# Performance work log

Hardware: AMD Instinct MI355X
Metric: run time of the kernel (lower is better)

The kernel has to match this reference:

```python
import jax, jax.numpy as jnp
from jax import lax
import numpy as np

HIDDEN = 128  # ConvLSTM hidden channels


def _conv(x, w, b, stride):
    # torch Conv2d(kernel=3, padding=1), NCHW / OIHW
    y = lax.conv_general_dilated(x, w, stride, [(1, 1), (1, 1)],
                                 dimension_numbers=('NCHW', 'OIHW', 'NCHW'))
    return y + b[None, :, None, None]


def _convT(x, w, b):
    # torch ConvTranspose2d(k=3, stride=(2,1), padding=1, output_padding=(1,0))
    # torch weight layout [Cin, Cout, kH, kW] -> flip spatially, swap IO
    wf = jnp.flip(w, (2, 3)).transpose(1, 0, 2, 3)
    y = lax.conv_general_dilated(x, wf, (1, 1), [(1, 2), (1, 1)],
                                 lhs_dilation=(2, 1),
                                 dimension_numbers=('NCHW', 'OIHW', 'NCHW'))
    return y + b[None, :, None, None]


def _bn(x, g, be, m, v):
    # eval-mode BatchNorm2d, eps=1e-5
    return g[None, :, None, None] * (x - m[None, :, None, None]) * lax.rsqrt(v[None, :, None, None] + 1e-5) + be[None, :, None, None]


def _lrelu(x):
    return jnp.where(x >= 0, x, 0.2 * x)


def _convlstm(e5, w, b):
    # e5: [B, 256, F, T]; scan over time with h,c state of shape [B, HIDDEN, F, 1]
    B, C, F, T = e5.shape
    xs = jnp.moveaxis(e5, 3, 0)[..., None]  # [T, B, C, F, 1]
    h0 = jnp.zeros((B, HIDDEN, F, 1), e5.dtype)

    def step(carry, xt):
        h, c = carry
        gates = _conv(jnp.concatenate([xt, h], axis=1), w, b, (1, 1))  # [B, 4H, F, 1]
        i, f, o, g = jnp.split(gates, 4, axis=1)
        c = jax.nn.sigmoid(f) * c + jax.nn.sigmoid(i) * jnp.tanh(g)
        h = jax.nn.sigmoid(o) * jnp.tanh(c)
        return (h, c), h

    _, hs = lax.scan(step, (h0, h0), xs)  # hs: [T, B, H, F, 1]
    return jnp.moveaxis(hs[..., 0], 0, 3)  # [B, H, F, T]


def _forward(x, enc1_w, enc1_b, enc1_g, enc1_be, enc1_m, enc1_v, enc2_w, enc2_b, enc2_g, enc2_be, enc2_m, enc2_v, enc3_w, enc3_b, enc3_g, enc3_be, enc3_m, enc3_v, enc4_w, enc4_b, enc4_g, enc4_be, enc4_m, enc4_v, enc5_w, enc5_b, enc5_g, enc5_be, enc5_m, enc5_v, lstm_w, lstm_b, dec5_w, dec5_b, dec5_g, dec5_be, dec5_m, dec5_v, dec4_w, dec4_b, dec4_g, dec4_be, dec4_m, dec4_v, dec3_w, dec3_b, dec3_g, dec3_be, dec3_m, dec3_v, dec2_w, dec2_b, dec2_g, dec2_be, dec2_m, dec2_v, dec1_w, dec1_b):
    x_log = jnp.log10(x + 1e-8)
    e1 = _lrelu(_bn(_conv(x_log, enc1_w, enc1_b, (2, 1)), enc1_g, enc1_be, enc1_m, enc1_v))
    e2 = _lrelu(_bn(_conv(e1, enc2_w, enc2_b, (2, 1)), enc2_g, enc2_be, enc2_m, enc2_v))
    e3 = _lrelu(_bn(_conv(e2, enc3_w, enc3_b, (2, 1)), enc3_g, enc3_be, enc3_m, enc3_v))
    e4 = _lrelu(_bn(_conv(e3, enc4_w, enc4_b, (2, 1)), enc4_g, enc4_be, enc4_m, enc4_v))
    e5 = _lrelu(_bn(_conv(e4, enc5_w, enc5_b, (2, 1)), enc5_g, enc5_be, enc5_m, enc5_v))
    lstm_out = _convlstm(e5, lstm_w, lstm_b)  # [B, 128, 8, T]
    d5 = jax.nn.relu(_bn(_convT(lstm_out, dec5_w, dec5_b), dec5_g, dec5_be, dec5_m, dec5_v))
    d4 = jax.nn.relu(_bn(_convT(jnp.concatenate([d5, e4], 1), dec4_w, dec4_b), dec4_g, dec4_be, dec4_m, dec4_v))
    d3 = jax.nn.relu(_bn(_convT(jnp.concatenate([d4, e3], 1), dec3_w, dec3_b), dec3_g, dec3_be, dec3_m, dec3_v))
    d2 = jax.nn.relu(_bn(_convT(jnp.concatenate([d3, e2], 1), dec2_w, dec2_b), dec2_g, dec2_be, dec2_m, dec2_v))
    mask = jax.nn.sigmoid(_convT(jnp.concatenate([d2, e1], 1), dec1_w, dec1_b))
    return x * mask


def setup_inputs() -> dict:
    key = jax.random.key(0)
    ks = list(jax.random.split(key, 64))
    it = iter(ks)
    d = {}
    d['x'] = jax.random.uniform(next(it), (16, 1, 256, 512), jnp.float32)

    def conv_block(name, cin, cout, bn=True):
        d[name + '_w'] = jax.random.normal(next(it), (cout, cin, 3, 3), jnp.float32) * 0.05
        d[name + '_b'] = jnp.zeros((cout,), jnp.float32)
        if bn:
            d[name + '_g'] = jnp.ones((cout,), jnp.float32)
            d[name + '_be'] = jnp.zeros((cout,), jnp.float32)
            d[name + '_m'] = jax.random.normal(next(it), (cout,), jnp.float32) * 0.01
            d[name + '_v'] = jnp.ones((cout,), jnp.float32)

    def convT_block(name, cin, cout, bn=True):
        # torch ConvTranspose2d weight [Cin, Cout, kH, kW]
        d[name + '_w'] = jax.random.normal(next(it), (cin, cout, 3, 3), jnp.float32) * 0.05
        d[name + '_b'] = jnp.zeros((cout,), jnp.float32)
        if bn:
            d[name + '_g'] = jnp.ones((cout,), jnp.float32)
            d[name + '_be'] = jnp.zeros((cout,), jnp.float32)
            d[name + '_m'] = jax.random.normal(next(it), (cout,), jnp.float32) * 0.01
            d[name + '_v'] = jnp.ones((cout,), jnp.float32)

    for i, (ci, co) in enumerate([(1, 16), (16, 32), (32, 64), (64, 128), (128, 256)], start=1):
        conv_block(f'enc{i}', ci, co)
    d['lstm_w'] = jax.random.normal(next(it), (4 * HIDDEN, 256 + HIDDEN, 3, 3), jnp.float32) * 0.05
    d['lstm_b'] = jnp.zeros((4 * HIDDEN,), jnp.float32)
    convT_block('dec5', 128, 128)
    convT_block('dec4', 256, 64)
    convT_block('dec3', 128, 32)
    convT_block('dec2', 64, 16)
    convT_block('dec1', 32, 1, bn=False)
    return d


def reference(x, enc1_w, enc1_b, enc1_g, enc1_be, enc1_m, enc1_v, enc2_w, enc2_b, enc2_g, enc2_be, enc2_m, enc2_v, enc3_w, enc3_b, enc3_g, enc3_be, enc3_m, enc3_v, enc4_w, enc4_b, enc4_g, enc4_be, enc4_m, enc4_v, enc5_w, enc5_b, enc5_g, enc5_be, enc5_m, enc5_v, lstm_w, lstm_b, dec5_w, dec5_b, dec5_g, dec5_be, dec5_m, dec5_v, dec4_w, dec4_b, dec4_g, dec4_be, dec4_m, dec4_v, dec3_w, dec3_b, dec3_g, dec3_be, dec3_m, dec3_v, dec2_w, dec2_b, dec2_g, dec2_be, dec2_m, dec2_v, dec1_w, dec1_b):
    return _forward(x, enc1_w, enc1_b, enc1_g, enc1_be, enc1_m, enc1_v, enc2_w, enc2_b, enc2_g, enc2_be, enc2_m, enc2_v, enc3_w, enc3_b, enc3_g, enc3_be, enc3_m, enc3_v, enc4_w, enc4_b, enc4_g, enc4_be, enc4_m, enc4_v, enc5_w, enc5_b, enc5_g, enc5_be, enc5_m, enc5_v, lstm_w, lstm_b, dec5_w, dec5_b, dec5_g, dec5_be, dec5_m, dec5_v, dec4_w, dec4_b, dec4_g, dec4_be, dec4_m, dec4_v, dec3_w, dec3_b, dec3_g, dec3_be, dec3_m, dec3_v, dec2_w, dec2_b, dec2_g, dec2_be, dec2_m, dec2_v, dec1_w, dec1_b)
```

## Files before the change

### kernel.cpp

```cpp
#include <hip/hip_runtime.h>
#include <math.h>


#define WW 512
#define BB 16
#define TT 512

typedef unsigned short u16;
typedef __attribute__((ext_vector_type(8))) short bf16x8;
typedef __attribute__((ext_vector_type(4))) float f32x4;

__device__ __forceinline__ float sigm_(float x){ return 1.f/(1.f+__expf(-x)); }
__device__ __forceinline__ float tanh_(float x){ return 1.f - 2.f/(1.f+__expf(2.f*x)); }
__device__ __forceinline__ float b2f(u16 u){ return __uint_as_float(((unsigned)u)<<16); }
__device__ __forceinline__ u16 f2b(float f){
  unsigned x = __float_as_uint(f);
  return (u16)((x + 0x7fffu + ((x>>16)&1u)) >> 16);
}

__global__ void k_log10(const float* __restrict__ x, u16* __restrict__ y, int n){
  int i = blockIdx.x*256 + threadIdx.x;
  if (i < n) y[i] = f2b(log10f(x[i] + 1e-8f));
}

__global__ __launch_bounds__(128) void k_conv_enc(
    const u16* __restrict__ in, const float* __restrict__ w,
    const float* __restrict__ bias, const float* __restrict__ bg,
    const float* __restrict__ bb_, const float* __restrict__ bm,
    const float* __restrict__ bv, u16* __restrict__ out,
    int Cin, int Cout, int Hin, int Hout)
{
  int blk = blockIdx.x;
  int ho = blk % Hout; blk /= Hout;
  int co = blk % Cout; int b = blk / Cout;
  int t0 = threadIdx.x*4;
  float a0=0.f,a1=0.f,a2=0.f,a3=0.f;
  const float* wb = w + (size_t)co*Cin*9;
  for (int ci=0; ci<Cin; ++ci){
    const u16* ib = in + (size_t)(b*Cin+ci)*Hin*WW;
    const float* wc = wb + ci*9;
    #pragma unroll
    for (int kh=0; kh<3; ++kh){
      int hi = 2*ho + kh - 1;
      if (hi < 0 || hi >= Hin) continue;
      float w0 = wc[kh*3+0], w1 = wc[kh*3+1], w2 = wc[kh*3+2];
      const u16* row = ib + (size_t)hi*WW + t0;
      ushort4 xc = *(const ushort4*)row;
      float x0=b2f(xc.x), x1=b2f(xc.y), x2=b2f(xc.z), x3=b2f(xc.w);
      float xm = (t0==0)    ? 0.f : b2f(row[-1]);
      float xp = (t0+4>=WW) ? 0.f : b2f(row[4]);
      a0 += w0*xm + w1*x0 + w2*x1;
      a1 += w0*x0 + w1*x1 + w2*x2;
      a2 += w0*x1 + w1*x2 + w2*x3;
      a3 += w0*x2 + w1*x3 + w2*xp;
    }
  }
  float sc = bg[co]*rsqrtf(bv[co]+1e-5f);
  float sh = bb_[co] - bm[co]*sc + bias[co]*sc;
  float r0 = sc*a0+sh, r1 = sc*a1+sh, r2 = sc*a2+sh, r3 = sc*a3+sh;
  r0 = (r0>=0.f)?r0:0.2f*r0; r1 = (r1>=0.f)?r1:0.2f*r1;
  r2 = (r2>=0.f)?r2:0.2f*r2; r3 = (r3>=0.f)?r3:0.2f*r3;
  *(ushort4*)(out + ((size_t)((b*Cout+co)*Hout+ho))*WW + t0) =
      make_ushort4(f2b(r0), f2b(r1), f2b(r2), f2b(r3));
}

__global__ __launch_bounds__(256) void k_prep_enc(
    const float* __restrict__ w, const float* __restrict__ b,
    const float* __restrict__ g, const float* __restrict__ be,
    const float* __restrict__ m, const float* __restrict__ v,
    u16* __restrict__ A, float* __restrict__ bias2, int Cin, int Cout, int KPAD)
{
  int co = blockIdx.x;
  float sc = g[co]*rsqrtf(v[co]+1e-5f);
  if (threadIdx.x == 0) bias2[co] = be[co] - m[co]*sc + b[co]*sc;
  for (int idx = threadIdx.x; idx < 3*KPAD; idx += 256){
    int kw = idx / KPAD, k = idx - kw*KPAD;
    float val = 0.f;
    if (k < Cin*3){ int ci = k/3, kh = k - ci*3; val = w[(((size_t)co*Cin+ci)*3+kh)*3+kw]*sc; }
    A[(size_t)(kw*Cout+co)*KPAD + k] = f2b(val);
  }
}

__global__ __launch_bounds__(256) void k_prep_dec(
    const float* __restrict__ w, const float* __restrict__ b,
    const float* __restrict__ g, const float* __restrict__ be,
    const float* __restrict__ m, const float* __restrict__ v,
    u16* __restrict__ AE, u16* __restrict__ AO, float* __restrict__ bias2,
    int Cin, int Cout)
{
  int co = blockIdx.x;
  float sc = g[co]*rsqrtf(v[co]+1e-5f);
  if (threadIdx.x == 0) bias2[co] = be[co] - m[co]*sc + b[co]*sc;
  for (int idx = threadIdx.x; idx < 3*Cin; idx += 256){
    int kw = idx / Cin, ci = idx - kw*Cin;
    const float* wp = w + ((size_t)ci*Cout + co)*9;
    AE[(size_t)(kw*Cout+co)*Cin + ci]          = f2b(wp[3+kw]*sc);
    AO[((size_t)(kw*Cout+co)*Cin + ci)*2 + 0]  = f2b(wp[6+kw]*sc);
    AO[((size_t)(kw*Cout+co)*Cin + ci)*2 + 1]  = f2b(wp[0+kw]*sc);
  }
}

template<int MT,int NT,int WMW,int WNW,int C1,int C2,int COUT,int HIN,int MODE,int MTL>
__global__ __launch_bounds__(256,2) void k_conv_mfma(
    const u16* __restrict__ inA, const u16* __restrict__ inB,
    const u16* __restrict__ AE, const u16* __restrict__ AO,
    const float* __restrict__ bias2, u16* __restrict__ out)
{
  constexpr int CIN  = C1 + C2;
  constexpr int HOUT = MODE ? HIN*2 : HIN/2;
  constexpr int KPAD0 = MODE ? CIN : ((C1*3+31)/32)*32;
  constexpr int LDK = 40;
  __shared__ __align__(16) u16 sB[130*LDK];
  int bi = blockIdx.x;
  int tt = bi & 3; bi >>= 2;
  int mt0 = 0;
  if (MTL == 2){ mt0 = bi & 1; bi >>= 1; }
  int ho = bi % HOUT, b = bi / HOUT;
  int t0 = tt*128;
  int tid = threadIdx.x;
  int w = tid>>6, L = tid&63, q = L>>4, n = L&15;
  int wm = w / WNW, wn = w % WNW;
  int co_base = (mt0*WMW + wm)*MT*16;
  int no = wn*NT*16;
  int odd = MODE ? (ho & 1) : 0;
  int nch     = MODE ? (odd ? CIN/16 : CIN/32) : KPAD0/32;
  int kstride = MODE ? (odd ? 2*CIN : CIN) : KPAD0;
  const u16* Ap = (MODE && odd) ? AO : AE;
  int kloc = tid>>3, seg = tid&7;
  f32x4 cfr[MT][NT];
  #pragma unroll
  for (int mt=0; mt<MT; ++mt)
    #pragma unroll
    for (int nt=0; nt<NT; ++nt){ cfr[mt][nt][0]=0.f; cfr[mt][nt][1]=0.f; cfr[mt][nt][2]=0.f; cfr[mt][nt][3]=0.f; }

  for (int kk=0; kk<nch; ++kk){
    int k = kk*32 + kloc;
    const u16* src = nullptr;
    if (MODE == 0){
      int ci = k/3, kh = k - 3*ci;
      int hi = 2*ho + kh - 1;
      if (k < C1*3 && hi >= 0 && hi < HIN)
        src = inA + ((size_t)(b*C1+ci)*HIN + hi)*WW;
    } else {
      int ci, hi;
      if (!odd){ ci = k; hi = ho>>1; }
      else { ci = k>>1; hi = (k&1) ? ((ho+1)>>1) : ((ho-1)>>1); }
      if (hi < HIN)
        src = (ci < C1) ? inA + ((size_t)(b*C1+ci)*HIN + hi)*WW
                        : inB + ((size_t)(b*C2+(ci-C1))*HIN + hi)*WW;
    }
    uint4 va = make_uint4(0,0,0,0), vb = make_uint4(0,0,0,0);
    u16 hl = 0, hr = 0;
    if (src){
      const u16* p = src + t0 + seg*16;
      va = *(const uint4*)p; vb = *(const uint4*)(p+8);
      if (seg==0 && t0 > 0)      hl = src[t0-1];
      if (seg==1 && t0+128 < WW) hr = src[t0+128];
    }
    __syncthreads();
    {
      const u16* s = (const u16*)&va;
      #pragma unroll
      for (int c=0;c<8;++c){ int vv=(c+seg)&7; sB[(1+seg*16+vv)*LDK + kloc] = s[vv]; }
      s = (const u16*)&vb;
      #pragma unroll
      for (int c=0;c<8;++c){ int vv=(c+seg)&7; sB[(9+seg*16+vv)*LDK + kloc] = s[vv]; }
      if (seg==0) sB[0*LDK + kloc]   = hl;
      if (seg==1) sB[129*LDK + kloc] = hr;
    }
    __syncthreads();
    #pragma unroll
    for (int kw=0; kw<3; ++kw){
      int tsh = MODE ? (2-kw) : kw;
      bf16x8 bfr[NT];
      #pragma unroll
      for (int nt=0; nt<NT; ++nt)
        bfr[nt] = *(const bf16x8*)(sB + (size_t)(no + nt*16 + n + tsh)*LDK + q*8);
      #pragma unroll
      for (int mt=0; mt<MT; ++mt){
        bf16x8 a = *(const bf16x8*)(Ap + ((size_t)(kw*COUT) + co_base + mt*16 + n)*kstride + kk*32 + q*8);
        #pragma unroll
        for (int nt=0; nt<NT; ++nt)
          cfr[mt][nt] = __builtin_amdgcn_mfma_f32_16x16x32_bf16(a, bfr[nt], cfr[mt][nt], 0,0,0);
      }
    }
  }
  #pragma unroll
  for (int mt=0; mt<MT; ++mt){
    #pragma unroll
    for (int r=0; r<4; ++r){
      int co = co_base + mt*16 + q*4 + r;
      float bs = bias2[co];
      #pragma unroll
      for (int nt=0; nt<NT; ++nt){
        float vv = cfr[mt][nt][r] + bs;
        vv = MODE ? fmaxf(vv, 0.f) : ((vv>=0.f)?vv:0.2f*vv);
        int t = t0 + no + nt*16 + n;
        out[((size_t)(b*COUT+co)*HOUT + ho)*WW + t] = f2b(vv);
      }
    }
  }
}

__global__ __launch_bounds__(256) void k_prep_w(
    const float* __restrict__ lstm_w, u16* __restrict__ Wxb, u16* __restrict__ Whb)
{
  int co = blockIdx.x;
  for (int k = threadIdx.x; k < 1152; k += 256){
    if (k < 768){
      int ci = k/3, kf = k - ci*3;
      Wxb[(size_t)co*768 + k] = f2b(lstm_w[((size_t)co*384 + ci)*9 + kf*3 + 1]);
    } else {
      int kh = k - 768;
      int ci = kh/3, kf = kh - ci*3;
      Whb[(size_t)co*384 + kh] = f2b(lstm_w[((size_t)co*384 + 256 + ci)*9 + kf*3 + 1]);
    }
  }
}

__global__ __launch_bounds__(256,3) void k_xconv_mfma(
    const u16* __restrict__ e5, const u16* __restrict__ Wxb,
    const float* __restrict__ bias, u16* __restrict__ gt)
{
  __shared__ __align__(16) u16 smem[128*136];
  int bi = blockIdx.x;
  int tt = bi & 3, cot = (bi>>2) & 3, f = (bi>>4) & 7, b = bi>>7;
  int tid = threadIdx.x, w = tid>>6, L = tid&63, q = L>>4, n = L&15;
  int co_off = (w>>1)*64, t_off = (w&1)*64;
  int sr = tid>>3, sseg = tid&7;
  f32x4 cfr[4][4];
  #pragma unroll
  for (int i=0;i<4;++i)
    #pragma unroll
    for (int j=0;j<4;++j){ cfr[i][j][0]=0.f; cfr[i][j][1]=0.f; cfr[i][j][2]=0.f; cfr[i][j][3]=0.f; }
  const u16* e5b = e5 + (size_t)b*256*8*WW + tt*128 + sseg*16;
  const u16* ap0 = Wxb + (size_t)(cot*128 + co_off + n)*768 + q*8;

  for (int kk=0; kk<24; ++kk){
    int k0 = kk*32;
    {
      int k = k0 + sr;
      int ci = k/3, kf = k - ci*3, fi = f + kf - 1;
      union { uint4 v[2]; u16 s[16]; } uu;
      if (fi >= 0 && fi < 8){
        const u16* src = e5b + ((size_t)ci*8 + fi)*WW;
        uu.v[0] = *(const uint4*)src;
        uu.v[1] = *(const uint4*)(src+8);
      } else {
        uu.v[0] = make_uint4(0,0,0,0); uu.v[1] = make_uint4(0,0,0,0);
      }
      __syncthreads();
      #pragma unroll
      for (int c=0;c<16;++c){ int vv=(c+sseg)&15; smem[(sseg*16+vv)*40 + sr] = uu.s[vv]; }
    }
    __syncthreads();
    bf16x8 bfr[4];
    #pragma unroll
    for (int nt=0; nt<4; ++nt)
      bfr[nt] = *(const bf16x8*)(smem + (size_t)(t_off + nt*16 + n)*40 + q*8);
    #pragma unroll
    for (int mt=0; mt<4; ++mt){
      bf16x8 a = *(const bf16x8*)(ap0 + (size_t)mt*16*768 + k0);
      #pragma unroll
      for (int nt=0; nt<4; ++nt)
        cfr[mt][nt] = __builtin_amdgcn_mfma_f32_16x16x32_bf16(a, bfr[nt], cfr[mt][nt], 0,0,0);
    }
  }
  __syncthreads();
  #pragma unroll
  for (int mt=0; mt<4; ++mt){
    #pragma unroll
    for (int r2=0; r2<2; ++r2){
      int co_l = co_off + mt*16 + q*4 + r2*2;
      float bs0 = bias[cot*128 + co_l], bs1 = bias[cot*128 + co_l + 1];
      #pragma unroll
      for (int nt=0; nt<4; ++nt){
        int t_l = t_off + nt*16 + n;
        float v0 = cfr[mt][nt][r2*2]   + bs0;
        float v1 = cfr[mt][nt][r2*2+1] + bs1;
        unsigned pk = (unsigned)f2b(v0) | ((unsigned)f2b(v1)<<16);
        *(unsigned*)(smem + (size_t)t_l*136 + co_l) = pk;
      }
    }
  }
  __syncthreads();
  int row0 = tid>>6, lane2 = tid&63;
  size_t gbase = (((size_t)b*512 + tt*128)*8 + f)*512 + cot*128;
  for (int p=0; p<32; ++p){
    int t_l = p*4 + row0;
    unsigned v = *(const unsigned*)(smem + (size_t)t_l*136 + lane2*2);
    *(unsigned*)(gt + gbase + (size_t)t_l*8*512 + lane2*2) = v;
  }
}

__global__ __launch_bounds__(512,2) void k_lstm_scan(
    const u16* __restrict__ gt, const u16* __restrict__ Whb,
    u16* __restrict__ hs)
{
  __shared__ __align__(16) u16 Bl[6144+16];
  __shared__ float Gl[512*9];
  int b = blockIdx.x;
  int tid = threadIdx.x, w = tid>>6, L = tid&63, q = L>>4, n = L&15;
  int ch = tid>>2, fa = tid&3, fb = fa|4;
  for (int i = tid; i < 6144+16; i += 512) Bl[i] = 0;
  bf16x8 afr[48];
  #pragma unroll
  for (int mt=0; mt<4; ++mt){
    const u16* ap = Whb + (size_t)(w*64 + mt*16 + n)*384 + q*8;
    #pragma unroll
    for (int kt=0; kt<12; ++kt)
      afr[mt*12+kt] = *(const bf16x8*)(ap + kt*32);
  }
  int sa[6];
  #pragma unroll
  for (int i2=0;i2<2;++i2){
    int fi = i2 ? fb : fa;
    #pragma unroll
    for (int kf=0;kf<3;++kf){
      int ff = fi + 1 - kf;
      int k = ch*3 + kf;
      sa[i2*3+kf] = (ff>=0 && ff<8)
          ? (((k>>5)*4 + ((k>>3)&3))*128 + ff*8 + (k&7))
          : (6144 + (tid&7));
    }
  }
  float c0 = 0.f, c1 = 0.f;
  __syncthreads();
  const size_t gbase = (size_t)b*512;
  const u16* pa = gt + gbase*4096 + fa*512 + ch;
  const u16* pb = gt + gbase*4096 + fb*512 + ch;
  u16 gc[8];
  #pragma unroll
  for (int g=0; g<4; ++g){ gc[g] = pa[g*128]; gc[4+g] = pb[g*128]; }
  for (int t=0; t<TT; ++t){
    u16 gn[8];
    {
      int tc = (t+1 < TT) ? (t+1) : t;
      const u16* qa = pa + (size_t)tc*4096;
      const u16* qb = pb + (size_t)tc*4096;
      #pragma unroll
      for (int g=0; g<4; ++g){ gn[g] = qa[g*128]; gn[4+g] = qb[g*128]; }
    }
    f32x4 cfr[4];
    #pragma unroll
    for (int mt=0; mt<4; ++mt){ cfr[mt][0]=0.f; cfr[mt][1]=0.f; cfr[mt][2]=0.f; cfr[mt][3]=0.f; }
    #pragma unroll
    for (int kt=0; kt<12; ++kt){
      bf16x8 bfr = *(const bf16x8*)(Bl + ((kt*4+q)*16 + n)*8);
      #pragma unroll
      for (int mt=0; mt<4; ++mt)
        cfr[mt] = __builtin_amdgcn_mfma_f32_16x16x32_bf16(afr[mt*12+kt], bfr, cfr[mt], 0,0,0);
    }
    if (n < 8){
      #pragma unroll
      for (int mt=0; mt<4; ++mt){
        int co = w*64 + mt*16 + q*4;
        #pragma unroll
        for (int r=0; r<4; ++r) Gl[(co+r)*9 + n] = cfr[mt][r];
      }
    }
    __syncthreads();
    float i0 = Gl[ ch      *9 + fa] + b2f(gc[0]);
    float f0 = Gl[(128+ch)*9 + fa] + b2f(gc[1]);
    float o0 = Gl[(256+ch)*9 + fa] + b2f(gc[2]);
    float g0 = Gl[(384+ch)*9 + fa] + b2f(gc[3]);
    float i1 = Gl[ ch      *9 + fb] + b2f(gc[4]);
    float f1 = Gl[(128+ch)*9 + fb] + b2f(gc[5]);
    float o1 = Gl[(256+ch)*9 + fb] + b2f(gc[6]);
    float g1 = Gl[(384+ch)*9 + fb] + b2f(gc[7]);
    c0 = sigm_(f0)*c0 + sigm_(i0)*tanh_(g0);
    c1 = sigm_(f1)*c1 + sigm_(i1)*tanh_(g1);
    float h0 = sigm_(o0)*tanh_(c0);
    float h1 = sigm_(o1)*tanh_(c1);
    u16 hb0 = f2b(h0), hb1 = f2b(h1);
    u16* op = hs + ((gbase + t)*128 + ch)*8;
    op[fa] = hb0;
    op[fb] = hb1;
    Bl[sa[0]] = hb0; Bl[sa[1]] = hb0; Bl[sa[2]] = hb0;
    Bl[sa[3]] = hb1; Bl[sa[4]] = hb1; Bl[sa[5]] = hb1;
    __syncthreads();
    #pragma unroll
    for (int g=0; g<8; ++g) gc[g] = gn[g];
  }
}

__global__ __launch_bounds__(256) void k_transpose_u16(
    const u16* __restrict__ in, u16* __restrict__ out, int R, int C)
{
  __shared__ u16 tile[32][33];
  int b = blockIdx.z;
  const u16* ip = in  + (size_t)b*R*C;
  u16*       op = out + (size_t)b*R*C;
  int c0 = blockIdx.x*32, r0 = blockIdx.y*32;
  #pragma unroll
  for (int i = threadIdx.y; i < 32; i += 8)
    tile[i][threadIdx.x] = ip[(size_t)(r0+i)*C + (c0+threadIdx.x)];
  __syncthreads();
  #pragma unroll
  for (int i = threadIdx.y; i < 32; i += 8)
    op[(size_t)(c0+i)*R + (r0+threadIdx.x)] = tile[threadIdx.x][i];
}

__global__ __launch_bounds__(128) void k_convT(
    const u16* __restrict__ inA, int C1,
    const u16* __restrict__ inB, int C2,
    const float* __restrict__ w, const float* __restrict__ bias,
    const float* __restrict__ xorig, float* __restrict__ fout,
    int Cout, int Hin)
{
  int Hout = Hin*2;
  int blk = blockIdx.x;
  int y = blk % Hout; blk /= Hout;
  int co = blk % Cout; int b = blk / Cout;
  int t0 = threadIdx.x*4;
  int Cin = C1 + C2;
  int kh0, hi0, kh1 = -1, hi1 = 0;
  if ((y&1)==0){ kh0 = 1; hi0 = y>>1; }
  else { kh0 = 2; hi0 = (y-1)>>1; int h1 = (y+1)>>1; if (h1 < Hin){ kh1 = 0; hi1 = h1; } }
  float a0=0.f,a1=0.f,a2=0.f,a3=0.f;
  for (int ci=0; ci<Cin; ++ci){
    const u16* ib = (ci<C1) ? inA + (size_t)(b*C1+ci)*Hin*WW
                            : inB + (size_t)(b*C2+(ci-C1))*Hin*WW;
    const float* wc = w + ((size_t)ci*Cout + co)*9;
    {
      float w0 = wc[kh0*3+0], w1 = wc[kh0*3+1], w2 = wc[kh0*3+2];
      const u16* row = ib + (size_t)hi0*WW + t0;
      ushort4 xc = *(const ushort4*)row;
      float x0=b2f(xc.x), x1=b2f(xc.y), x2=b2f(xc.z), x3=b2f(xc.w);
      float xm = (t0==0)    ? 0.f : b2f(row[-1]);
      float xp = (t0+4>=WW) ? 0.f : b2f(row[4]);
      a0 += w2*xm + w1*x0 + w0*x1;
      a1 += w2*x0 + w1*x1 + w0*x2;
      a2 += w2*x1 + w1*x2 + w0*x3;
      a3 += w2*x2 + w1*x3 + w0*xp;
    }
    if (kh1 >= 0){
      float w0 = wc[0], w1 = wc[1], w2 = wc[2];
      const u16* row = ib + (size_t)hi1*WW + t0;
      ushort4 xc = *(const ushort4*)row;
      float x0=b2f(xc.x), x1=b2f(xc.y), x2=b2f(xc.z), x3=b2f(xc.w);
      float xm = (t0==0)    ? 0.f : b2f(row[-1]);
      float xp = (t0+4>=WW) ? 0.f : b2f(row[4]);
      a0 += w2*xm + w1*x0 + w0*x1;
      a1 += w2*x0 + w1*x1 + w0*x2;
      a2 += w2*x1 + w1*x2 + w0*x3;
      a3 += w2*x2 + w1*x3 + w0*xp;
    }
  }
  size_t opos = ((size_t)((b*Cout+co)*Hout + y))*WW + t0;
  float bi = bias[co];
  const float4 xv = *(const float4*)(xorig + ((size_t)(b*256 + y))*WW + t0);
  float4 o;
  o.x = xv.x * sigm_(a0+bi); o.y = xv.y * sigm_(a1+bi);
  o.z = xv.z * sigm_(a2+bi); o.w = xv.w * sigm_(a3+bi);
  *(float4*)(fout + opos) = o;
}

extern "C" void kernel_launch(void* const* d_in, const int* in_sizes, int n_in,
                              void* d_out, int out_size, void* d_ws, size_t ws_size,
                              hipStream_t stream) {
  const float* x = (const float*)d_in[0];
  struct Blk { const float *w,*b,*g,*be,*m,*v; };
  auto grab = [&](int p){ return Blk{ (const float*)d_in[p], (const float*)d_in[p+1],
                                      (const float*)d_in[p+2], (const float*)d_in[p+3],
                                      (const float*)d_in[p+4], (const float*)d_in[p+5] }; };
  Blk enc1 = grab(1), enc2 = grab(7), enc3 = grab(13), enc4 = grab(19), enc5 = grab(25);
  const float* lstm_w = (const float*)d_in[31];
  const float* lstm_b = (const float*)d_in[32];
  Blk dec5 = grab(33), dec4 = grab(39), dec3 = grab(45), dec2 = grab(51);
  const float* dec1_w = (const float*)d_in[57];
  const float* dec1_b = (const float*)d_in[58];

  char* ws = (char*)d_ws;
  #define MBOF(x) ((size_t)(x)*1048576ULL)
  u16*   xlog = (u16*)  (ws + MBOF(0));
  u16*   Wxb  = (u16*)  (ws + MBOF(0));
  u16*   Whb  = (u16*)  (ws + MBOF(1));
  char*  P0   =          ws + 1572864;
  u16*   e1   = (u16*)  (ws + MBOF(4));
  u16*   e2   = (u16*)  (ws + MBOF(36));
  u16*   e3   = (u16*)  (ws + MBOF(68));
  u16*   e4   = (u16*)  (ws + MBOF(100));
  u16*   e5   = (u16*)  (ws + MBOF(132));
  u16*   hst  = (u16*)  (ws + MBOF(132));
  u16*   lout = (u16*)  (ws + MBOF(148));
  u16*   gt   = (u16*)  (ws + MBOF(164));
  u16*   d5   = (u16*)  (ws + MBOF(164));
  u16*   d4   = (u16*)  (ws + MBOF(132));
  u16*   d3   = (u16*)  (ws + MBOF(196));
  u16*   d2   = (u16*)  (ws + MBOF(164));

  u16* encA2 = (u16*)(P0 + 0);       u16* encA3 = (u16*)(P0 + 12288);
  u16* encA4 = (u16*)(P0 + 49152);   u16* encA5 = (u16*)(P0 + 196608);
  u16* decE5 = (u16*)(P0 + 786432);  u16* decO5 = (u16*)(P0 + 884736);
  u16* decE4 = (u16*)(P0 + 1081344); u16* decO4 = (u16*)(P0 + 1179648);
  u16* decE3 = (u16*)(P0 + 1376256); u16* decO3 = (u16*)(P0 + 1400832);
  u16* decE2 = (u16*)(P0 + 1449984); u16* decO2 = (u16*)(P0 + 1456128);
  float* bE2 = (float*)(P0 + 1468416); float* bE3 = (float*)(P0 + 1469440);
  float* bE4 = (float*)(P0 + 1470464); float* bE5 = (float*)(P0 + 1471488);
  float* bD5 = (float*)(P0 + 1472512); float* bD4 = (float*)(P0 + 1473536);
  float* bD3 = (float*)(P0 + 1474560); float* bD2 = (float*)(P0 + 1475584);

  { int n = BB*256*WW; k_log10<<<(n+255)/256, 256, 0, stream>>>(x, xlog, n); }
  k_conv_enc<<<BB*16*128, 128, 0, stream>>>(xlog, enc1.w, enc1.b, enc1.g, enc1.be, enc1.m, enc1.v, e1, 1, 16, 256, 128);
  k_prep_w<<<512, 256, 0, stream>>>(lstm_w, Wxb, Whb);
  k_prep_enc<<<32,  256, 0, stream>>>(enc2.w, enc2.b, enc2.g, enc2.be, enc2.m, enc2.v, encA2, bE2, 16, 32, 64);
  k_prep_enc<<<64,  256, 0, stream>>>(enc3.w, enc3.b, enc3.g, enc3.be, enc3.m, enc3.v, encA3, bE3, 32, 64, 96);
  k_prep_enc<<<128, 256, 0, stream>>>(enc4.w, enc4.b, enc4.g, enc4.be, enc4.m, enc4.v, encA4, bE4, 64, 128, 192);
  k_prep_enc<<<256, 256, 0, stream>>>(enc5.w, enc5.b, enc5.g, enc5.be, enc5.m, enc5.v, encA5, bE5, 128, 256, 384);
  k_prep_dec<<<128, 256, 0, stream>>>(dec5.w, dec5.b, dec5.g, dec5.be, dec5.m, dec5.v, decE5, decO5, bD5, 128, 128);
  k_prep_dec<<<64,  256, 0, stream>>>(dec4.w, dec4.b, dec4.g, dec4.be, dec4.m, dec4.v, decE4, decO4, bD4, 256, 64);
  k_prep_dec<<<32,  256, 0, stream>>>(dec3.w, dec3.b, dec3.g, dec3.be, dec3.m, dec3.v, decE3, decO3, bD3, 128, 32);
  k_prep_dec<<<16,  256, 0, stream>>>(dec2.w, dec2.b, dec2.g, dec2.be, dec2.m, dec2.v, decE2, decO2, bD2, 64, 16);
  k_conv_mfma<2,2,1,4, 16,0, 32,128,0,1><<<BB*64*4,   256, 0, stream>>>(e1, e1, encA2, encA2, bE2, e2);
  k_conv_mfma<4,2,1,4, 32,0, 64, 64,0,1><<<BB*32*4,   256, 0, stream>>>(e2, e2, encA3, encA3, bE3, e3);
  k_conv_mfma<4,4,2,2, 64,0,128, 32,0,1><<<BB*16*4,   256, 0, stream>>>(e3, e3, encA4, encA4, bE4, e4);
  k_conv_mfma<4,4,2,2,128,0,256, 16,0,2><<<BB*8*2*4,  256, 0, stream>>>(e4, e4, encA5, encA5, bE5, e5);
  k_xconv_mfma<<<BB*8*16, 256, 0, stream>>>(e5, Wxb, lstm_b, gt);
  k_lstm_scan<<<BB, 512, 0, stream>>>(gt, Whb, hst);
  k_transpose_u16<<<dim3(1024/32, 512/32, BB), dim3(32,8), 0, stream>>>(hst, lout, 512, 1024);
  k_conv_mfma<4,4,2,2,128,  0,128,  8,1,1><<<BB*16*4,  256, 0, stream>>>(lout, lout, decE5, decO5, bD5, d5);
  k_conv_mfma<4,2,1,4,128,128, 64, 16,1,1><<<BB*32*4,  256, 0, stream>>>(d5, e4, decE4, decO4, bD4, d4);
  k_conv_mfma<2,2,1,4, 64, 64, 32, 32,1,1><<<BB*64*4,  256, 0, stream>>>(d4, e3, decE3, decO3, bD3, d3);
  k_conv_mfma<1,2,1,4, 32, 32, 16, 64,1,1><<<BB*128*4, 256, 0, stream>>>(d3, e2, decE2, decO2, bD2, d2);
  k_convT<<<BB*1*256, 128, 0, stream>>>(d2, 16, e1, 16, dec1_w, dec1_b, x, (float*)d_out, 1, 128);
}
```

Before: 2.351 ms.

## Remap LSTM scan so gate math runs in MFMA registers with double-buffered h

Each wave's weight rows are remapped so that one wave holds all four gates (i,f,o,g) for the same channels in its MFMA accumulators. The LSTM cell update can then happen straight from registers, without the Gl shared-memory round trip. The h state now uses a double-buffered LDS array, which cuts the two block barriers per timestep to one lightweight lgkmcnt+s_barrier. The encoder conv loop also drops one __syncthreads per k-iteration by moving the barrier to the end of the loop body. Only half the lanes (n<8) do the gate math, which concentrates the transcendental work, and occupancy hint drops to 1 block per SM.

```diff
diff --git a/kernel.cpp b/kernel.cpp
--- a/kernel.cpp
+++ b/kernel.cpp
@@ -16,6 +16,9 @@
 __device__ __forceinline__ u16 f2b(float f){
   unsigned x = __float_as_uint(f);
   return (u16)((x + 0x7fffu + ((x>>16)&1u)) >> 16);
+}
+__device__ __forceinline__ void bar_lds(){
+  asm volatile("s_waitcnt lgkmcnt(0)\n\ts_barrier" ::: "memory");
 }
 
 __global__ void k_log10(const float* __restrict__ x, u16* __restrict__ y, int n){
@@ -249,7 +252,6 @@
       } else {
         uu.v[0] = make_uint4(0,0,0,0); uu.v[1] = make_uint4(0,0,0,0);
       }
-      __syncthreads();
       #pragma unroll
       for (int c=0;c<16;++c){ int vv=(c+sseg)&15; smem[(sseg*16+vv)*40 + sr] = uu.s[vv]; }
     }
@@ -265,8 +267,8 @@
       for (int nt=0; nt<4; ++nt)
         cfr[mt][nt] = __builtin_amdgcn_mfma_f32_16x16x32_bf16(a, bfr[nt], cfr[mt][nt], 0,0,0);
     }
-  }
-  __syncthreads();
+    __syncthreads();
+  }
   #pragma unroll
   for (int mt=0; mt<4; ++mt){
     #pragma unroll
@@ -293,94 +295,79 @@
   }
 }
 
-__global__ __launch_bounds__(512,2) void k_lstm_scan(
+__global__ __launch_bounds__(512,1) void k_lstm_scan(
     const u16* __restrict__ gt, const u16* __restrict__ Whb,
     u16* __restrict__ hs)
 {
-  __shared__ __align__(16) u16 Bl[6144+16];
-  __shared__ float Gl[512*9];
+  __shared__ __align__(16) u16 Bl[2*6144 + 16];
   int b = blockIdx.x;
   int tid = threadIdx.x, w = tid>>6, L = tid&63, q = L>>4, n = L&15;
-  int ch = tid>>2, fa = tid&3, fb = fa|4;
-  for (int i = tid; i < 6144+16; i += 512) Bl[i] = 0;
-  bf16x8 afr[48];
+  for (int i = tid; i < 2*6144+16; i += 512) Bl[i] = 0;
+  bf16x8 afr[4][12];
   #pragma unroll
   for (int mt=0; mt<4; ++mt){
-    const u16* ap = Whb + (size_t)(w*64 + mt*16 + n)*384 + q*8;
-    #pragma unroll
-    for (int kt=0; kt<12; ++kt)
-      afr[mt*12+kt] = *(const bf16x8*)(ap + kt*32);
-  }
-  int sa[6];
-  #pragma unroll
-  for (int i2=0;i2<2;++i2){
-    int fi = i2 ? fb : fa;
+    const u16* ap = Whb + (size_t)(mt*128 + w*16 + n)*384 + q*8;
+    #pragma unroll
+    for (int kt=0; kt<12; ++kt) afr[mt][kt] = *(const bf16x8*)(ap + kt*32);
+  }
+  int chb = w*16 + q*4;
+  int sa[12];
+  #pragma unroll
+  for (int r=0;r<4;++r)
     #pragma unroll
     for (int kf=0;kf<3;++kf){
-      int ff = fi + 1 - kf;
-      int k = ch*3 + kf;
-      sa[i2*3+kf] = (ff>=0 && ff<8)
-          ? (((k>>5)*4 + ((k>>3)&3))*128 + ff*8 + (k&7))
-          : (6144 + (tid&7));
-    }
-  }
-  float c0 = 0.f, c1 = 0.f;
+      int ff = n + 1 - kf;
+      int k = (chb + r)*3 + kf;
+      sa[r*3+kf] = (n<8 && ff>=0 && ff<8)
+        ? ((k>>5)*512 + ((k>>3)&3)*128 + ff*8 + (k&7))
+        : (2*6144 + (tid&15));
+    }
+  float cst[4] = {0.f,0.f,0.f,0.f};
+  const u16* gp = gt + (size_t)b*512*4096 + n*512 + chb;
+  u16* hp = hs + ((size_t)b*512 * 128 + chb)*8 + n;
+  ushort4 ga[4], gb[4];
+  #pragma unroll
+  for (int mt=0;mt<4;++mt) ga[mt] = *(const ushort4*)(gp + mt*128);
   __syncthreads();
-  const size_t gbase = (size_t)b*512;
-  const u16* pa = gt + gbase*4096 + fa*512 + ch;
-  const u16* pb = gt + gbase*4096 + fb*512 + ch;
-  u16 gc[8];
-  #pragma unroll
-  for (int g=0; g<4; ++g){ gc[g] = pa[g*128]; gc[4+g] = pb[g*128]; }
+  int pb = 0;
   for (int t=0; t<TT; ++t){
-    u16 gn[8];
     {
-      int tc = (t+1 < TT) ? (t+1) : t;
-      const u16* qa = pa + (size_t)tc*4096;
-      const u16* qb = pb + (size_t)tc*4096;
-      #pragma unroll
-      for (int g=0; g<4; ++g){ gn[g] = qa[g*128]; gn[4+g] = qb[g*128]; }
-    }
+      int tc = (t+1<TT)? t+1 : t;
+      const u16* gq = gp + (size_t)tc*4096;
+      #pragma unroll
+      for (int mt=0;mt<4;++mt) gb[mt] = *(const ushort4*)(gq + mt*128);
+    }
+    const u16* Bp = Bl + pb*6144;
     f32x4 cfr[4];
     #pragma unroll
-    for (int mt=0; mt<4; ++mt){ cfr[mt][0]=0.f; cfr[mt][1]=0.f; cfr[mt][2]=0.f; cfr[mt][3]=0.f; }
+    for (int mt=0;mt<4;++mt){ cfr[mt][0]=0.f; cfr[mt][1]=0.f; cfr[mt][2]=0.f; cfr[mt][3]=0.f; }
     #pragma unroll
     for (int kt=0; kt<12; ++kt){
-      bf16x8 bfr = *(const bf16x8*)(Bl + ((kt*4+q)*16 + n)*8);
-      #pragma unroll
-      for (int mt=0; mt<4; ++mt)
-        cfr[mt] = __builtin_amdgcn_mfma_f32_16x16x32_bf16(afr[mt*12+kt], bfr, cfr[mt], 0,0,0);
-    }
+      bf16x8 bfr = *(const bf16x8*)(Bp + ((kt*4+q)*16 + n)*8);
+      #pragma unroll
+      for (int mt=0;mt<4;++mt)
+        cfr[mt] = __builtin_amdgcn_mfma_f32_16x16x32_bf16(afr[mt][kt], bfr, cfr[mt], 0,0,0);
+    }
+    u16* Bw = Bl + (pb^1)*6144;
     if (n < 8){
       #pragma unroll
-      for (int mt=0; mt<4; ++mt){
-        int co = w*64 + mt*16 + q*4;
-        #pragma unroll
-        for (int r=0; r<4; ++r) Gl[(co+r)*9 + n] = cfr[mt][r];
+      for (int r=0;r<4;++r){
+        float gi = cfr[0][r] + b2f(((const u16*)&ga[0])[r]);
+        float gf = cfr[1][r] + b2f(((const u16*)&ga[1])[r]);
+        float go = cfr[2][r] + b2f(((const u16*)&ga[2])[r]);
+        float gg = cfr[3][r] + b2f(((const u16*)&ga[3])[r]);
+        float c = sigm_(gf)*cst[r] + sigm_(gi)*tanh_(gg);
+        cst[r] = c;
+        float h = sigm_(go)*tanh_(c);
+        u16 hb = f2b(h);
+        hp[(size_t)t*1024 + r*8] = hb;
+        Bw[sa[r*3+0]] = hb; Bw[sa[r*3+1]] = hb; Bw[sa[r*3+2]] = hb;
       }
     }
-    __syncthreads();
-    float i0 = Gl[ ch      *9 + fa] + b2f(gc[0]);
-    float f0 = Gl[(128+ch)*9 + fa] + b2f(gc[1]);
-    float o0 = Gl[(256+ch)*9 + fa] + b2f(gc[2]);
-    float g0 = Gl[(384+ch)*9 + fa] + b2f(gc[3]);
-    float i1 = Gl[ ch      *9 + fb] + b2f(gc[4]);
-    float f1 = Gl[(128+ch)*9 + fb] + b2f(gc[5]);
-    float o1 = Gl[(256+ch)*9 + fb] + b2f(gc[6]);
-    float g1 = Gl[(384+ch)*9 + fb] + b2f(gc[7]);
-    c0 = sigm_(f0)*c0 + sigm_(i0)*tanh_(g0);
-    c1 = sigm_(f1)*c1 + sigm_(i1)*tanh_(g1);
-    float h0 = sigm_(o0)*tanh_(c0);
-    float h1 = sigm_(o1)*tanh_(c1);
-    u16 hb0 = f2b(h0), hb1 = f2b(h1);
-    u16* op = hs + ((gbase + t)*128 + ch)*8;
-    op[fa] = hb0;
-    op[fb] = hb1;
-    Bl[sa[0]] = hb0; Bl[sa[1]] = hb0; Bl[sa[2]] = hb0;
-    Bl[sa[3]] = hb1; Bl[sa[4]] = hb1; Bl[sa[5]] = hb1;
-    __syncthreads();
-    #pragma unroll
-    for (int g=0; g<8; ++g) gc[g] = gn[g];
+    bar_lds();
+    #pragma unroll
+    for (int mt=0;mt<4;++mt) ga[mt] = gb[mt];
+    pb ^= 1;
   }
 }
 
```

Measured after the change: 2.477 ms. 1.05x slower.
